# Performance work log

Measured on AMD Instinct MI355X. Metric: run time of the kernel, lower is better.

The kernel has to match this reference:

```python
import jax, jax.numpy as jnp
import numpy as np

# Static module configuration (matches init_kwargs)
NLAT, NLON = 256, 256
LMAX = 128            # max_degree
MMAX = 129            # nlon//2 + 1 == max_degree + 1
CIN, COUT, BATCH = 32, 32, 8
NUM_COEFFS = 2 * LMAX * MMAX  # real+imag flattened, = 33024


def _cc_quadrature(n):
    """Clenshaw-Curtis nodes (colatitudes incl. poles) and weights on [-1,1]."""
    N = n - 1
    tj = np.pi * np.arange(n) / N
    k = np.arange(1, N // 2 + 1)
    bk = np.where(2 * k == N, 1.0, 2.0)
    S = np.cos(2.0 * np.outer(tj, k)) @ (bk / (4.0 * k * k - 1.0))
    c = np.full(n, 2.0)
    c[0] = c[-1] = 1.0
    w = (c / N) * (1.0 - S)
    return tj, w


def _legpoly(mmax, lmax, t):
    """Orthonormal associated Legendre P_l^m(cos t) incl. 1/sqrt(4pi) and CS phase.
    Returns array [mmax, lmax, nlat]; entries with l < m are zero."""
    ct, st = np.cos(t), np.sin(t)
    p = np.zeros((mmax, lmax, t.shape[0]))
    p[0, 0] = 1.0 / np.sqrt(4.0 * np.pi)
    for m in range(1, min(mmax, lmax)):
        p[m, m] = -np.sqrt((2.0 * m + 1.0) / (2.0 * m)) * st * p[m - 1, m - 1]
    for m in range(min(mmax, lmax)):
        if m + 1 < lmax:
            p[m, m + 1] = np.sqrt(2.0 * m + 3.0) * ct * p[m, m]
    for m in range(mmax):
        for l in range(m + 2, lmax):
            a = np.sqrt((4.0 * l * l - 1.0) / (l * l - m * m))
            b = np.sqrt(((l - 1.0) ** 2 - m * m) / (4.0 * (l - 1.0) ** 2 - 1.0))
            p[m, l] = a * (ct * p[m, l - 1] - b * p[m, l - 2])
    return p


_T, _WQ = _cc_quadrature(NLAT)
_PCT_NP = _legpoly(MMAX, LMAX, _T)                 # synthesis Legendre matrix
_PCT = jnp.asarray(_PCT_NP, jnp.float32)           # [mmax, lmax, nlat]
_PCTW = jnp.asarray(_PCT_NP * _WQ[None, None, :], jnp.float32)  # analysis (quadrature weighted)


def setup_inputs() -> dict:
    key = jax.random.key(0)
    k1, k2 = jax.random.split(key)
    x = jax.random.normal(k1, (BATCH, CIN, NLAT, NLON), jnp.float32)
    scale = (1.0 / (CIN * COUT * NUM_COEFFS)) ** 0.5
    weight = scale * jax.random.normal(k2, (CIN, COUT, NUM_COEFFS), jnp.float32)
    return {"x": x, "weight": weight}


def reference(x, weight):
    B, C = x.shape[0], x.shape[1]
    # ---- forward real SHT (ortho norm, equiangular / Clenshaw-Curtis) ----
    # longitudinal rfft with 'forward' norm, scaled by 2*pi
    xh = (2.0 * np.pi / NLON) * jnp.fft.rfft(x, axis=-1)   # [B,C,nlat,nlon//2+1] complex
    xh = xh[..., :MMAX]
    re = jnp.einsum('bckm,mlk->bclm', jnp.real(xh), _PCTW)  # [B,C,lmax,mmax]
    im = jnp.einsum('bckm,mlk->bclm', jnp.imag(xh), _PCTW)
    spec = jnp.stack([re, im], axis=-1).reshape(B, C, NUM_COEFFS)
    # ---- spectral channel mixing: per-coefficient dense channel mix ----
    out = jnp.einsum('bix,iox->box', spec, weight)          # [B,Cout,NUM_COEFFS]
    out = out.reshape(B, COUT, LMAX, MMAX, 2)
    # ---- inverse real SHT ----
    rr = jnp.einsum('bolm,mlk->bokm', out[..., 0], _PCT)    # [B,Cout,nlat,mmax]
    ri = jnp.einsum('bolm,mlk->bokm', out[..., 1], _PCT)
    Xm = jax.lax.complex(rr, ri)                            # mmax == nlon//2+1
    y = jnp.fft.irfft(Xm, n=NLON, axis=-1) * NLON           # irfft norm='forward'
    return y
```

## Files before the change

### kernel.cpp

```cpp
#include <hip/hip_runtime.h>


typedef __attribute__((ext_vector_type(8))) short short8;
typedef __attribute__((ext_vector_type(4))) float f32x4;

__device__ __forceinline__ ushort bf16_rtn(float v) {
  uint u = __float_as_uint(v);
  return (ushort)((u + 0x7FFFu + ((u >> 16) & 1u)) >> 16);
}
__device__ __forceinline__ void split2(float v, ushort& h, ushort& l) {
  h = bf16_rtn(v);
  float hf = __uint_as_float(((uint)h) << 16);
  l = bf16_rtn(v - hf);
}

__global__ __launch_bounds__(256) void k_tables(
    ushort* __restrict__ Th, ushort* __restrict__ Tl,
    ushort* __restrict__ TiTh, ushort* __restrict__ TiTl,
    ushort* __restrict__ PWh, ushort* __restrict__ PWl,
    ushort* __restrict__ PTh, ushort* __restrict__ PTl) {
  const double PI = 3.14159265358979323846264338327950288;
  const int t = threadIdx.x;
  const int m = blockIdx.x;
  __shared__ double sCos[256];
  __shared__ double sCoef[128];
  __shared__ double sRatio[128];
  __shared__ double sA[128], sB[128];

  if (m == 128) {
    const double scale = 2.0 * PI / 256.0;
    sCos[t] = cos(scale * (double)t);
    __syncthreads();
    const int n = t;
    for (int ch = 0; ch < 8; ++ch) {
      uint th16[16], tl16[16];
#pragma unroll
      for (int j = 0; j < 16; ++j) {
        const int mm = ch * 16 + j;
        const int r = (mm * n) & 255;
        const double c = sCos[r];
        const double s = sCos[(r + 192) & 255];
        const double wm = (mm == 0) ? 1.0 : 2.0;
        ushort h, l;
        split2((float)(scale * c), h, l);  Th[(2*mm)*256+n]=h;   Tl[(2*mm)*256+n]=l;
        split2((float)(-scale * s), h, l); Th[(2*mm+1)*256+n]=h; Tl[(2*mm+1)*256+n]=l;
        ushort h2, l2b, h3, l3;
        split2((float)(wm * c), h2, l2b);
        split2((float)(-wm * s), h3, l3);
        th16[j] = (uint)h2 | ((uint)h3 << 16);
        tl16[j] = (uint)l2b | ((uint)l3 << 16);
      }
      const int base = n * 256 + ch * 32;
#pragma unroll
      for (int q4 = 0; q4 < 4; ++q4) {
        *(uint4*)(TiTh + base + q4 * 8) = make_uint4(th16[4*q4], th16[4*q4+1], th16[4*q4+2], th16[4*q4+3]);
        *(uint4*)(TiTl + base + q4 * 8) = make_uint4(tl16[4*q4], tl16[4*q4+1], tl16[4*q4+2], tl16[4*q4+3]);
      }
    }
    return;
  }

  const double scale255 = 2.0 * PI / 255.0;
  if (t < 255) sCos[t] = cos(scale255 * (double)t);
  if (t >= 1 && t < 128) {
    const double dt = (double)t;
    sCoef[t]  = 2.0 / (4.0 * dt * dt - 1.0);
    sRatio[t] = (2.0 * dt + 1.0) / (2.0 * dt);
    if (t >= m + 2) {
      const double dl = dt, dm = (double)m;
      sA[t] = sqrt((4.0*dl*dl - 1.0) / (dl*dl - dm*dm));
      sB[t] = sqrt(((dl-1.0)*(dl-1.0) - dm*dm) / (4.0*(dl-1.0)*(dl-1.0) - 1.0));
    }
  }
  __syncthreads();

  const int k = t;
  const double tj = PI * (double)k / 255.0;
  double ssum = 0.0;
  {
    int r = 0;
    for (int kk = 1; kk <= 127; ++kk) {
      r += k; if (r >= 255) r -= 255;
      ssum += sCoef[kk] * sCos[r];
    }
  }
  const double cj = (k == 0 || k == 255) ? 1.0 : 2.0;
  const double wq = cj / 255.0 * (1.0 - ssum);
  const double ct = cos(tj), st = sin(tj);
  double prod = 1.0, stp = 1.0;
  for (int mm = 1; mm <= m; ++mm) { prod *= sRatio[mm]; stp *= -st; }
  const double pmm = (1.0 / sqrt(4.0 * PI)) * sqrt(prod) * stp;
  const double sq2m3 = sqrt(2.0 * (double)m + 3.0);

  const size_t pwB = (size_t)m * 32768;
  const size_t ptB = (size_t)m * 32768 + (size_t)k * 128;
  double plm1 = 0.0, plm2 = 0.0;
  for (int lc0 = 0; lc0 < 128; lc0 += 16) {
    uint hq[8], lq[8];
#pragma unroll
    for (int j = 0; j < 16; ++j) {
      const int l = lc0 + j;
      double val;
      if (l < m)           val = 0.0;
      else if (l == m)     val = pmm;
      else if (l == m + 1) val = sq2m3 * ct * pmm;
      else                 val = sA[l] * (ct * plm1 - sB[l] * plm2);
      plm2 = plm1; plm1 = val;
      ushort h, lo; split2((float)val, h, lo);
      if ((j & 1) == 0) { hq[j>>1] = (uint)h; lq[j>>1] = (uint)lo; }
      else              { hq[j>>1] |= ((uint)h) << 16; lq[j>>1] |= ((uint)lo) << 16; }
      ushort hw, lw; split2((float)(val * wq), hw, lw);
      PWh[pwB + (size_t)l * 256 + k] = hw;
      PWl[pwB + (size_t)l * 256 + k] = lw;
    }
    *(uint4*)(PTh + ptB + lc0)     = make_uint4(hq[0], hq[1], hq[2], hq[3]);
    *(uint4*)(PTh + ptB + lc0 + 8) = make_uint4(hq[4], hq[5], hq[6], hq[7]);
    *(uint4*)(PTl + ptB + lc0)     = make_uint4(lq[0], lq[1], lq[2], lq[3]);
    *(uint4*)(PTl + ptB + lc0 + 8) = make_uint4(lq[4], lq[5], lq[6], lq[7]);
  }
}

template<int AM, int BM, int CM>
__global__ __launch_bounds__(256) void mfma_gemm(
    const ushort* __restrict__ Ah, const ushort* __restrict__ Al, const float* __restrict__ Af,
    const ushort* __restrict__ Bh, const ushort* __restrict__ Bl, const float* __restrict__ Bf,
    float* __restrict__ C, ushort* __restrict__ Ch, ushort* __restrict__ Cl,
    int lda, int ldb, int ldc, int K,
    long aZ, int aShift, long bZ, int bShift, long cZ, int cColOff,
    int kFromZ, int mSkipFromZ)
{
  __shared__ __align__(16) short sAh[128*40];
  __shared__ __align__(16) short sAl[128*40];
  __shared__ __align__(16) short sBh[128*40];
  __shared__ __align__(16) short sBl[128*40];
  const int z = blockIdx.z;
  const long aOff = ((long)(z >> aShift)) * aZ;
  const long bOff = ((long)(z >> bShift)) * bZ;
  const long cOff = (long)z * cZ;
  const int i0 = blockIdx.y * 128;
  const int j0 = blockIdx.x * 128;
  const int t = threadIdx.x;
  const int lane = t & 63, w = t >> 6;
  const int wy = w >> 1, wx = w & 1;
  const int il = lane & 15, q = lane >> 4;
  const int kstart = kFromZ ? ((z >> 1) & ~31) : 0;
  const int nsk = mSkipFromZ ? ((z >> 1) >> 4) : 0;

  f32x4 acc[4][4];
#pragma unroll
  for (int a = 0; a < 4; ++a)
#pragma unroll
    for (int b = 0; b < 4; ++b) acc[a][b] = (f32x4){0.f, 0.f, 0.f, 0.f};

  for (int k0 = kstart; k0 < K; k0 += 32) {
    __syncthreads();
    if constexpr (AM == 0) {
      const int r = t >> 1, ks = (t & 1) * 16;
      const size_t g = (size_t)aOff + (size_t)(i0 + r) * lda + k0 + ks;
      *(short8*)&sAh[r*40+ks]   = *(const short8*)(Ah + g);
      *(short8*)&sAh[r*40+ks+8] = *(const short8*)(Ah + g + 8);
      *(short8*)&sAl[r*40+ks]   = *(const short8*)(Al + g);
      *(short8*)&sAl[r*40+ks+8] = *(const short8*)(Al + g + 8);
    } else {
      const int kk0 = 8*w + 2*q;
      const float* s0 = Af + aOff + (size_t)(k0 + kk0) * lda + i0 + il;
      const float* s1 = s0 + lda;
#pragma unroll
      for (int c = 0; c < 8; ++c) {
        float v0 = s0[c*16], v1 = s1[c*16];
        ushort h0,l0,h1,l1; split2(v0,h0,l0); split2(v1,h1,l1);
        const int idx = (il + 16*c)*40 + kk0;
        *(uint*)&sAh[idx] = (uint)h0 | ((uint)h1 << 16);
        *(uint*)&sAl[idx] = (uint)l0 | ((uint)l1 << 16);
      }
    }
    if constexpr (BM == 0) {
      const int r = t >> 1, ks = (t & 1) * 16;
      const size_t g = (size_t)bOff + (size_t)(j0 + r) * ldb + k0 + ks;
      *(short8*)&sBh[r*40+ks]   = *(const short8*)(Bh + g);
      *(short8*)&sBh[r*40+ks+8] = *(const short8*)(Bh + g + 8);
      *(short8*)&sBl[r*40+ks]   = *(const short8*)(Bl + g);
      *(short8*)&sBl[r*40+ks+8] = *(const short8*)(Bl + g + 8);
    } else {
      const int r = t >> 1, ks = (t & 1) * 16;
      const float* src = Bf + bOff + (size_t)(j0 + r) * ldb + k0 + ks;
#pragma unroll
      for (int jj = 0; jj < 4; ++jj) {
        float4 f = *(const float4*)(src + 4*jj);
        ushort h0,l0,h1,l1,h2,l2,h3,l3;
        split2(f.x,h0,l0); split2(f.y,h1,l1); split2(f.z,h2,l2); split2(f.w,h3,l3);
        *(ushort4*)&sBh[r*40+ks+4*jj] = make_ushort4(h0,h1,h2,h3);
        *(ushort4*)&sBl[r*40+ks+4*jj] = make_ushort4(l0,l1,l2,l3);
      }
    }
    __syncthreads();
    short8 afh[4], afl[4];
#pragma unroll
    for (int mi = 0; mi < 4; ++mi) {
      if (wy*4 + mi >= nsk) {
        const int row = wy*64 + mi*16 + il;
        afh[mi] = *(const short8*)&sAh[row*40 + q*8];
        afl[mi] = *(const short8*)&sAl[row*40 + q*8];
      }
    }
#pragma unroll
    for (int nj = 0; nj < 4; ++nj) {
      const int row = wx*64 + nj*16 + il;
      short8 bfh = *(const short8*)&sBh[row*40 + q*8];
      short8 bfl = *(const short8*)&sBl[row*40 + q*8];
#pragma unroll
      for (int mi = 0; mi < 4; ++mi) {
        if (wy*4 + mi >= nsk) {
          acc[mi][nj] = __builtin_amdgcn_mfma_f32_16x16x32_bf16(afh[mi], bfh, acc[mi][nj], 0, 0, 0);
          acc[mi][nj] = __builtin_amdgcn_mfma_f32_16x16x32_bf16(afh[mi], bfl, acc[mi][nj], 0, 0, 0);
          acc[mi][nj] = __builtin_amdgcn_mfma_f32_16x16x32_bf16(afl[mi], bfh, acc[mi][nj], 0, 0, 0);
        }
      }
    }
  }
#pragma unroll
  for (int mi = 0; mi < 4; ++mi)
#pragma unroll
    for (int nj = 0; nj < 4; ++nj)
#pragma unroll
      for (int r = 0; r < 4; ++r) {
        const long gi = i0 + wy*64 + mi*16 + q*4 + r;
        const long gj = j0 + wx*64 + nj*16 + il;
        if constexpr (CM == 0) {
          C[cOff + gi*ldc + cColOff + gj] = acc[mi][nj][r];
        } else {
          ushort h, lo; split2(acc[mi][nj][r], h, lo);
          const size_t idx = (size_t)(cOff + gi*ldc + cColOff + gj);
          Ch[idx] = h; Cl[idx] = lo;
        }
      }
}

__global__ __launch_bounds__(256) void k_stagec(const float* __restrict__ spec,
                                                const float* __restrict__ w,
                                                float* __restrict__ outb) {
  const int cb = blockIdx.x, l = blockIdx.y;
  if (cb * 16 > l) return;
  __shared__ float s_spec[32 * 257];
  __shared__ float s_w[256 * 33];
  const int t = threadIdx.x;
  const int c = t & 31, og = t >> 5;
  const size_t x0 = 258u * l + cb * 32;
  for (int cc = 0; cc < 32; ++cc)
    s_spec[cc * 257 + t] = spec[(size_t)(cb * 32 + cc) * 32768 + l * 256 + t];
  float acc[8][4] = {{0.f}};
  const int lr = t >> 4;
  const int lq = (t & 15) * 2;
  for (int isub = 0; isub < 4; ++isub) {
    __syncthreads();
    for (int pass = 0; pass < 16; ++pass) {
      const int rho = pass * 16 + lr;
      const int io = (isub * 8 + (rho >> 5)) * 32 + (rho & 31);
      const float2 wv = *(const float2*)&w[(size_t)io * 33024 + x0 + lq];
      s_w[rho * 33 + lq]     = wv.x;
      s_w[rho * 33 + lq + 1] = wv.y;
    }
    __syncthreads();
#pragma unroll
    for (int idp = 0; idp < 4; ++idp) {
      const int i0 = isub * 8 + idp * 2;
      const int r0 = idp * 64;
      float2 sv[8];
#pragma unroll
      for (int b = 0; b < 8; ++b)
        sv[b] = *(const float2*)&s_spec[c * 257 + b * 32 + i0];
      float wv0[4], wv1[4];
#pragma unroll
      for (int od = 0; od < 4; ++od) {
        wv0[od] = s_w[(r0 + og * 4 + od) * 33 + c];
        wv1[od] = s_w[(r0 + 32 + og * 4 + od) * 33 + c];
      }
#pragma unroll
      for (int b = 0; b < 8; ++b)
#pragma unroll
        for (int od = 0; od < 4; ++od)
          acc[b][od] = fmaf(sv[b].x, wv0[od], fmaf(sv[b].y, wv1[od], acc[b][od]));
    }
  }
  __syncthreads();
#pragma unroll
  for (int b = 0; b < 8; ++b)
#pragma unroll
    for (int od = 0; od < 4; ++od)
      s_w[c * 257 + b * 32 + og * 4 + od] = acc[b][od];
  __syncthreads();
  for (int cc = 0; cc < 32; ++cc)
    outb[(size_t)(cb * 32 + cc) * 32768 + l * 256 + t] = s_w[cc * 257 + t];
}

extern "C" void kernel_launch(void* const* d_in, const int* in_sizes, int n_in,
                              void* d_out, int out_size, void* d_ws, size_t ws_size,
                              hipStream_t stream) {
  const float* x = (const float*)d_in[0];
  const float* w = (const float*)d_in[1];
  float* y = (float*)d_out;
  char* ws = (char*)d_ws;

  ushort* Th   = (ushort*)(ws + 0);
  ushort* Tl   = (ushort*)(ws + 131072);
  ushort* TiTh = (ushort*)(ws + 262144);
  ushort* TiTl = (ushort*)(ws + 393216);
  ushort* PWh  = (ushort*)(ws + 524288);
  ushort* PWl  = (ushort*)(ws + 8912896);
  ushort* PTh  = (ushort*)(ws + 17301504);
  ushort* PTl  = (ushort*)(ws + 25690112);
  ushort* XHh  = (ushort*)(ws + 34078720);
  ushort* XHl  = (ushort*)(ws + 67633152);
  float* XM    = (float*)(ws + 34078720);
  float* spec  = (float*)(ws + 101187584);
  float* outb  = spec;

  k_tables<<<dim3(129), dim3(256), 0, stream>>>(Th, Tl, TiTh, TiTl, PWh, PWl, PTh, PTl);

  mfma_gemm<0,1,1><<<dim3(512, 2, 1), dim3(256), 0, stream>>>(
      Th, Tl, nullptr, nullptr, nullptr, x, nullptr, XHh, XHl,
      256, 256, 65536, 256, 0L, 0, 0L, 0, 0L, 0, 0, 0);

  mfma_gemm<0,0,0><<<dim3(2, 1, 256), dim3(256), 0, stream>>>(
      PWh, PWl, nullptr, XHh, XHl, nullptr, spec, nullptr, nullptr,
      256, 256, 256, 256, 32768L, 1, 65536L, 0, 32768L, 0, 0, 1);

  k_stagec<<<dim3(8, 128), dim3(256), 0, stream>>>(spec, w, outb);

  mfma_gemm<2,0,0><<<dim3(2, 2, 256), dim3(256), 0, stream>>>(
      nullptr, nullptr, outb, PTh, PTl, nullptr, XM, nullptr, nullptr,
      256, 128, 256, 128, 32768L, 0, 32768L, 1, 65536L, 0, 1, 0);

  mfma_gemm<2,0,0><<<dim3(2, 512, 1), dim3(256), 0, stream>>>(
      nullptr, nullptr, XM, TiTh, TiTl, nullptr, y, nullptr, nullptr,
      65536, 256, 256, 256, 0L, 0, 0L, 0, 0L, 0, 0, 0);
}
```

Measured before the change: 414.7 us.

## Load bf16 GEMM tiles directly into LDS with XOR-swizzled layout

Replaces the register-staged global-to-shared copies for the pre-split bf16 operands with direct global_load_lds 16-byte transfers. Drops the padded 40-element row stride in favour of a 32-element stride with an XOR swizzle on 8-element chunks, so the MFMA fragment reads and the fp32 split paths stay bank-conflict free. The aim is to cut VGPR traffic and LDS footprint in the loader. The risk is that the direct-to-LDS writes bypass the waits the compiler normally inserts, so synchronisation must still cover them, and the swizzle indexing has to match on both the write and read sides.

After: 410.2 us. No clear change (-1.1%).

```diff
diff --git a/kernel.cpp b/kernel.cpp
--- a/kernel.cpp
+++ b/kernel.cpp
@@ -12,6 +12,11 @@
   h = bf16_rtn(v);
   float hf = __uint_as_float(((uint)h) << 16);
   l = bf16_rtn(v - hf);
+}
+__device__ __forceinline__ void gl2lds16(const ushort* g, short* l) {
+  __builtin_amdgcn_global_load_lds(
+      (const __attribute__((address_space(1))) unsigned int*)g,
+      (__attribute__((address_space(3))) unsigned int*)l, 16, 0, 0);
 }
 
 __global__ __launch_bounds__(256) void k_tables(
@@ -129,10 +134,10 @@
     long aZ, int aShift, long bZ, int bShift, long cZ, int cColOff,
     int kFromZ, int mSkipFromZ)
 {
-  __shared__ __align__(16) short sAh[128*40];
-  __shared__ __align__(16) short sAl[128*40];
-  __shared__ __align__(16) short sBh[128*40];
-  __shared__ __align__(16) short sBl[128*40];
+  __shared__ __align__(16) short sAh[128*32];
+  __shared__ __align__(16) short sAl[128*32];
+  __shared__ __align__(16) short sBh[128*32];
+  __shared__ __align__(16) short sBl[128*32];
   const int z = blockIdx.z;
   const long aOff = ((long)(z >> aShift)) * aZ;
   const long bOff = ((long)(z >> bShift)) * bZ;
@@ -145,6 +150,9 @@
   const int il = lane & 15, q = lane >> 4;
   const int kstart = kFromZ ? ((z >> 1) & ~31) : 0;
   const int nsk = mSkipFromZ ? ((z >> 1) >> 4) : 0;
+  const int grow0 = w * 32 + (lane >> 2);
+  const int gchunk0 = (lane & 3) ^ ((lane >> 3) & 3);
+  const int cq = q ^ ((il >> 1) & 3);
 
   f32x4 acc[4][4];
 #pragma unroll
@@ -155,42 +163,53 @@
   for (int k0 = kstart; k0 < K; k0 += 32) {
     __syncthreads();
     if constexpr (AM == 0) {
-      const int r = t >> 1, ks = (t & 1) * 16;
-      const size_t g = (size_t)aOff + (size_t)(i0 + r) * lda + k0 + ks;
-      *(short8*)&sAh[r*40+ks]   = *(const short8*)(Ah + g);
-      *(short8*)&sAh[r*40+ks+8] = *(const short8*)(Ah + g + 8);
-      *(short8*)&sAl[r*40+ks]   = *(const short8*)(Al + g);
-      *(short8*)&sAl[r*40+ks+8] = *(const short8*)(Al + g + 8);
+#pragma unroll
+      for (int inst = 0; inst < 2; ++inst) {
+        const int r = grow0 + inst * 16;
+        const size_t g = (size_t)aOff + (size_t)(i0 + r) * lda + k0 + gchunk0 * 8;
+        short* dA = &sAh[(w * 32 + inst * 16) * 32];
+        short* dAl = &sAl[(w * 32 + inst * 16) * 32];
+        gl2lds16(Ah + g, dA);
+        gl2lds16(Al + g, dAl);
+      }
     } else {
       const int kk0 = 8*w + 2*q;
+      const int cbase = kk0 >> 3, koff = kk0 & 7;
       const float* s0 = Af + aOff + (size_t)(k0 + kk0) * lda + i0 + il;
       const float* s1 = s0 + lda;
 #pragma unroll
       for (int c = 0; c < 8; ++c) {
         float v0 = s0[c*16], v1 = s1[c*16];
         ushort h0,l0,h1,l1; split2(v0,h0,l0); split2(v1,h1,l1);
-        const int idx = (il + 16*c)*40 + kk0;
+        const int row = il + 16*c;
+        const int idx = row*32 + ((cbase ^ ((row>>1)&3)) << 3) + koff;
         *(uint*)&sAh[idx] = (uint)h0 | ((uint)h1 << 16);
         *(uint*)&sAl[idx] = (uint)l0 | ((uint)l1 << 16);
       }
     }
     if constexpr (BM == 0) {
-      const int r = t >> 1, ks = (t & 1) * 16;
-      const size_t g = (size_t)bOff + (size_t)(j0 + r) * ldb + k0 + ks;
-      *(short8*)&sBh[r*40+ks]   = *(const short8*)(Bh + g);
-      *(short8*)&sBh[r*40+ks+8] = *(const short8*)(Bh + g + 8);
-      *(short8*)&sBl[r*40+ks]   = *(const short8*)(Bl + g);
-      *(short8*)&sBl[r*40+ks+8] = *(const short8*)(Bl + g + 8);
+#pragma unroll
+      for (int inst = 0; inst < 2; ++inst) {
+        const int r = grow0 + inst * 16;
+        const size_t g = (size_t)bOff + (size_t)(j0 + r) * ldb + k0 + gchunk0 * 8;
+        short* dB = &sBh[(w * 32 + inst * 16) * 32];
+        short* dBl = &sBl[(w * 32 + inst * 16) * 32];
+        gl2lds16(Bh + g, dB);
+        gl2lds16(Bl + g, dBl);
+      }
     } else {
-      const int r = t >> 1, ks = (t & 1) * 16;
-      const float* src = Bf + bOff + (size_t)(j0 + r) * ldb + k0 + ks;
+      const int rr = t >> 1, ks = (t & 1) * 16;
+      const int rsw = (rr >> 1) & 3;
+      const float* src = Bf + bOff + (size_t)(j0 + rr) * ldb + k0 + ks;
 #pragma unroll
       for (int jj = 0; jj < 4; ++jj) {
         float4 f = *(const float4*)(src + 4*jj);
         ushort h0,l0,h1,l1,h2,l2,h3,l3;
         split2(f.x,h0,l0); split2(f.y,h1,l1); split2(f.z,h2,l2); split2(f.w,h3,l3);
-        *(ushort4*)&sBh[r*40+ks+4*jj] = make_ushort4(h0,h1,h2,h3);
-        *(ushort4*)&sBl[r*40+ks+4*jj] = make_ushort4(l0,l1,l2,l3);
+        const int pos = ks + 4*jj;
+        const int idx = rr*32 + ((((pos >> 3) ^ rsw)) << 3) + (pos & 7);
+        *(ushort4*)&sBh[idx] = make_ushort4(h0,h1,h2,h3);
+        *(ushort4*)&sBl[idx] = make_ushort4(l0,l1,l2,l3);
       }
     }
     __syncthreads();
@@ -199,15 +218,15 @@
     for (int mi = 0; mi < 4; ++mi) {
       if (wy*4 + mi >= nsk) {
         const int row = wy*64 + mi*16 + il;
-        afh[mi] = *(const short8*)&sAh[row*40 + q*8];
-        afl[mi] = *(const short8*)&sAl[row*40 + q*8];
+        afh[mi] = *(const short8*)&sAh[row*32 + cq*8];
+        afl[mi] = *(const short8*)&sAl[row*32 + cq*8];
       }
     }
 #pragma unroll
     for (int nj = 0; nj < 4; ++nj) {
       const int row = wx*64 + nj*16 + il;
-      short8 bfh = *(const short8*)&sBh[row*40 + q*8];
-      short8 bfl = *(const short8*)&sBl[row*40 + q*8];
+      short8 bfh = *(const short8*)&sBh[row*32 + cq*8];
+      short8 bfl = *(const short8*)&sBl[row*32 + cq*8];
 #pragma unroll
       for (int mi = 0; mi < 4; ++mi) {
         if (wy*4 + mi >= nsk) {
```
